# Optimization experiments

Measured on AMD Instinct MI355X. Metric: run time of the kernel, lower is better.

Reference implementation:

```python
import jax, jax.numpy as jnp
import numpy as np

N, M1, M2, D, S0, S1 = 60000, 40000, 40000, 64, 10, 20

def setup_inputs() -> dict:
    key = jax.random.key(0)
    ks = jax.random.split(key, 10)
    return {
        "h0": jax.random.normal(ks[0], (N, D), jnp.float32),
        "h1": jax.random.normal(ks[1], (M1, D), jnp.float32),
        "h2": jax.random.normal(ks[2], (M2, D), jnp.float32),
        "nei0": jax.random.randint(ks[3], (N, S0), 0, M1),
        "nei1": jax.random.randint(ks[4], (N, S1), 0, M2),
        "att_w0": jax.random.normal(ks[5], (1, 2 * D), jnp.float32) * 0.15,
        "att_w1": jax.random.normal(ks[6], (1, 2 * D), jnp.float32) * 0.15,
        "fc_w": jax.random.normal(ks[7], (D, D), jnp.float32) * 0.15,
        "fc_b": jnp.zeros((D,), jnp.float32),
        "fus_att_w": jax.random.normal(ks[8], (1, D), jnp.float32) * 0.15,
        "glob_att": jax.random.normal(ks[9], (1, D), jnp.float32) * 0.15,
        "gate": jnp.float32(0.8),
    }

def _nei_att(nei, h, h_refer, att_w):
    # F.embedding gather: [N, S, D]
    nei_emb = h[nei]
    d = h.shape[-1]
    # concat([h_refer, nei_emb]) @ att.T == h_refer@a_ref + nei_emb@a_nei
    a_ref, a_nei = att_w[0, :d], att_w[0, d:]
    scores = (h_refer @ a_ref)[:, None] + nei_emb @ a_nei  # [N, S]
    scores = jax.nn.leaky_relu(scores, 0.01)
    w = jax.nn.softmax(scores, axis=1)  # softmax over neighbors
    return jnp.einsum('ns,nsd->nd', w, nei_emb)

def reference(h0, h1, h2, nei0, nei1, att_w0, att_w1, fc_w, fc_b, fus_att_w, glob_att, gate):
    # intra (per neighbor type) attention + elu
    e0 = jax.nn.elu(_nei_att(nei0, h1, h0, att_w0))
    e1 = jax.nn.elu(_nei_att(nei1, h2, h0, att_w1))
    # fus_att (inter-type semantic attention)
    def beta_of(e):
        sp = jnp.tanh(e @ fc_w.T + fc_b)
        return (sp @ fus_att_w[0]).mean()
    beta = jax.nn.softmax(jnp.stack([beta_of(e0), beta_of(e1)]))
    z_mc = beta[0] * e0 + beta[1] * e1
    # global encoder: softmax over all nodes of all types
    all_nodes = jnp.concatenate([h0, h1, h2], axis=0)
    s = (all_nodes @ glob_att[0]) / jnp.sqrt(jnp.float32(D))
    w = jax.nn.softmax(s, axis=0)[:, None]
    global_embed = (w * all_nodes).sum(axis=0)  # [D]
    # weighted gate fusion
    gv = jax.nn.sigmoid(gate)
    return gv * z_mc + (1.0 - gv) * global_embed
```

## Files before the change

kernel.cpp:

```cpp
#include <hip/hip_runtime.h>
#include <math.h>

#define N_NODES 60000
#define M1_N    40000
#define M2_N    40000
#define DD      64
#define S0_N    10
#define S1_N    20
#define R_TOTAL (N_NODES + M1_N + M2_N)
#define T_H0    (N_NODES / 16)
#define T_H1    (T_H0 + M1_N / 16)
#define T_ALL   (T_H1 + M2_N / 16)
#define PROJ_GRID 1024
#define BETA_GRID 512

typedef __attribute__((ext_vector_type(8))) short short8;
typedef __attribute__((ext_vector_type(4))) float f32x4;

__device__ __forceinline__ float wave_sum(float x) {
#pragma unroll
    for (int o = 32; o >= 1; o >>= 1) x += __shfl_xor(x, o, 64);
    return x;
}
__device__ __forceinline__ float bcast(float v, int l) {
    return __uint_as_float(__builtin_amdgcn_readlane(__float_as_uint(v), l));
}
__device__ __forceinline__ float tanh_fast(float x) {
    return 1.f - 2.f / (__expf(2.f * x) + 1.f);
}
__device__ __forceinline__ unsigned short f2bf(float x) {
    unsigned u = __float_as_uint(x);
    return (unsigned short)((u + 0x7FFFu + ((u >> 16) & 1u)) >> 16);
}
__device__ __forceinline__ float bf2f(unsigned short u) {
    return __uint_as_float(((unsigned)u) << 16);
}

__global__ __launch_bounds__(256) void k_proj(
    const float* __restrict__ h0, const float* __restrict__ h1, const float* __restrict__ h2,
    const float* __restrict__ aw0, const float* __restrict__ aw1, const float* __restrict__ gatt,
    float* __restrict__ part,
    float* __restrict__ p0r0, float* __restrict__ p0r1,
    float* __restrict__ p1, float* __restrict__ p2,
    unsigned short* __restrict__ h1bf, unsigned short* __restrict__ h2bf)
{
    __shared__ float s_wsum[64];
    __shared__ float s_se;
    __shared__ float s_es[4][16];
    const int tid = threadIdx.x, lane = tid & 63, wid = tid >> 6;
    if (tid < 64) s_wsum[tid] = 0.f;
    if (tid == 0) s_se = 0.f;
    __syncthreads();

    const int m = lane & 15, quad = lane >> 4;

    short8 b0, b1;
    {
        const float* vsel = 0;
        if (m == 1) vsel = aw0;
        else if (m == 2) vsel = aw1;
        else if (m == 3) vsel = aw0 + DD;
        else if (m == 4) vsel = aw1 + DD;
        else if (m == 0) vsel = gatt;
#pragma unroll
        for (int j = 0; j < 8; j++) {
            b0[j] = vsel ? (short)f2bf(vsel[quad * 8 + j]) : (short)0;
            b1[j] = vsel ? (short)f2bf(vsel[32 + quad * 8 + j]) : (short)0;
        }
    }

    float wacc0[8], wacc1[8];
#pragma unroll
    for (int j = 0; j < 8; j++) { wacc0[j] = 0.f; wacc1[j] = 0.f; }
    float r_se = 0.f;

    const int gw = blockIdx.x * 4 + wid, nw = gridDim.x * 4;
    for (int tile = gw; tile < T_ALL; tile += nw) {
        const float* src; int rbase, region;
        if (tile < T_H0)      { src = h0; rbase = tile * 16;          region = 0; }
        else if (tile < T_H1) { src = h1; rbase = (tile - T_H0) * 16; region = 1; }
        else                  { src = h2; rbase = (tile - T_H1) * 16; region = 2; }
        const int row = rbase + m;
        const float4* rpa = (const float4*)(src + (size_t)row * DD + quad * 8);
        const float4* rpb = (const float4*)(src + (size_t)row * DD + 32 + quad * 8);
        const float4 va = rpa[0], vb = rpa[1];
        const float4 vc = rpb[0], vd = rpb[1];

        short8 a0, a1;
        a0[0] = (short)f2bf(va.x); a0[1] = (short)f2bf(va.y);
        a0[2] = (short)f2bf(va.z); a0[3] = (short)f2bf(va.w);
        a0[4] = (short)f2bf(vb.x); a0[5] = (short)f2bf(vb.y);
        a0[6] = (short)f2bf(vb.z); a0[7] = (short)f2bf(vb.w);
        a1[0] = (short)f2bf(vc.x); a1[1] = (short)f2bf(vc.y);
        a1[2] = (short)f2bf(vc.z); a1[3] = (short)f2bf(vc.w);
        a1[4] = (short)f2bf(vd.x); a1[5] = (short)f2bf(vd.y);
        a1[6] = (short)f2bf(vd.z); a1[7] = (short)f2bf(vd.w);

        f32x4 c = {0.f, 0.f, 0.f, 0.f};
        c = __builtin_amdgcn_mfma_f32_16x16x32_bf16(a0, b0, c, 0, 0, 0);
        c = __builtin_amdgcn_mfma_f32_16x16x32_bf16(a1, b1, c, 0, 0, 0);

        if (m == 0) {
            float4 e4;
            e4.x = __expf(c[0] * 0.125f); e4.y = __expf(c[1] * 0.125f);
            e4.z = __expf(c[2] * 0.125f); e4.w = __expf(c[3] * 0.125f);
            *(float4*)&s_es[wid][quad * 4] = e4;
        }
        __builtin_amdgcn_wave_barrier();
        const float es = s_es[wid][m];
        r_se += es;
        wacc0[0] = fmaf(es, va.x, wacc0[0]); wacc0[1] = fmaf(es, va.y, wacc0[1]);
        wacc0[2] = fmaf(es, va.z, wacc0[2]); wacc0[3] = fmaf(es, va.w, wacc0[3]);
        wacc0[4] = fmaf(es, vb.x, wacc0[4]); wacc0[5] = fmaf(es, vb.y, wacc0[5]);
        wacc0[6] = fmaf(es, vb.z, wacc0[6]); wacc0[7] = fmaf(es, vb.w, wacc0[7]);
        wacc1[0] = fmaf(es, vc.x, wacc1[0]); wacc1[1] = fmaf(es, vc.y, wacc1[1]);
        wacc1[2] = fmaf(es, vc.z, wacc1[2]); wacc1[3] = fmaf(es, vc.w, wacc1[3]);
        wacc1[4] = fmaf(es, vd.x, wacc1[4]); wacc1[5] = fmaf(es, vd.y, wacc1[5]);
        wacc1[6] = fmaf(es, vd.z, wacc1[6]); wacc1[7] = fmaf(es, vd.w, wacc1[7]);

        if (region == 0) {
            if (m == 1) { float4 t = {c[0], c[1], c[2], c[3]}; *(float4*)(p0r0 + rbase + quad * 4) = t; }
            if (m == 2) { float4 t = {c[0], c[1], c[2], c[3]}; *(float4*)(p0r1 + rbase + quad * 4) = t; }
        } else if (region == 1) {
            if (m == 3) { float4 t = {c[0], c[1], c[2], c[3]}; *(float4*)(p1 + rbase + quad * 4) = t; }
            *(short8*)(h1bf + (size_t)row * DD + quad * 8) = a0;
            *(short8*)(h1bf + (size_t)row * DD + 32 + quad * 8) = a1;
        } else {
            if (m == 4) { float4 t = {c[0], c[1], c[2], c[3]}; *(float4*)(p2 + rbase + quad * 4) = t; }
            *(short8*)(h2bf + (size_t)row * DD + quad * 8) = a0;
            *(short8*)(h2bf + (size_t)row * DD + 32 + quad * 8) = a1;
        }
    }

    r_se *= 0.25f;
#pragma unroll
    for (int o = 1; o <= 8; o <<= 1) {
#pragma unroll
        for (int j = 0; j < 8; j++) {
            wacc0[j] += __shfl_xor(wacc0[j], o, 64);
            wacc1[j] += __shfl_xor(wacc1[j], o, 64);
        }
    }
    if (m == 0) {
#pragma unroll
        for (int j = 0; j < 8; j++) {
            atomicAdd(&s_wsum[quad * 8 + j],      wacc0[j]);
            atomicAdd(&s_wsum[32 + quad * 8 + j], wacc1[j]);
        }
    }
    const float se = wave_sum(r_se);
    if (lane == 0) atomicAdd(&s_se, se);
    __syncthreads();
    if (tid < 64) part[tid * PROJ_GRID + blockIdx.x] = s_wsum[tid];
    if (tid == 64) part[64 * PROJ_GRID + blockIdx.x] = s_se;
}

__global__ __launch_bounds__(256) void k_attn(
    const unsigned short* __restrict__ h1bf,
    const int* __restrict__ nei0, const int* __restrict__ nei1,
    const float* __restrict__ p0r0, const float* __restrict__ p0r1,
    const float* __restrict__ p1,
    unsigned short* __restrict__ e0bf, unsigned short* __restrict__ e1bf)
{
    const int tid = threadIdx.x, lane = tid & 63, wid = tid >> 6;
    const int sub = lane & 15, grp = lane >> 4;
    const bool grp0 = (lane < S0_N);
    const bool grp1 = (lane >= 32) && (lane < 32 + S1_N);
    const int gw = blockIdx.x * 4 + wid;
    const int nw = gridDim.x * 4;
    for (int n = gw; n < N_NODES; n += nw) {
        const float pr0 = p0r0[n];
        const float pr1 = p0r1[n];

        int idx = 0; float w = 0.f;
        if (grp0) idx = nei0[n * S0_N + lane];
        if (grp1) idx = nei1[n * S1_N + (lane - 32)] + M1_N;
        if (grp0 | grp1) {
            float sc = (grp0 ? pr0 : pr1) + p1[idx];
            sc = (sc >= 0.f) ? sc : 0.01f * sc;
            w = __expf(sc);
        }

        int r0[3], r1[5];
#pragma unroll
        for (int j = 0; j < 3; j++) r0[j] = __shfl(idx, 4 * j + grp, 64);
#pragma unroll
        for (int j = 0; j < 5; j++) r1[j] = __shfl(idx, 32 + 4 * j + grp, 64);

        ushort4 u0[3], u1[5];
#pragma unroll
        for (int j = 0; j < 3; j++)
            u0[j] = *(const ushort4*)(h1bf + r0[j] * DD + 4 * sub);
#pragma unroll
        for (int j = 0; j < 5; j++)
            u1[j] = *(const ushort4*)(h1bf + r1[j] * DD + 4 * sub);

        float sv = w;
#pragma unroll
        for (int o = 16; o >= 1; o >>= 1) sv += __shfl_xor(sv, o, 64);
        const float inv0 = 1.f / bcast(sv, 0);
        const float inv1 = 1.f / bcast(sv, 32);

        float w0[3], w1[5];
#pragma unroll
        for (int j = 0; j < 3; j++) w0[j] = __shfl(w, 4 * j + grp, 64);
#pragma unroll
        for (int j = 0; j < 5; j++) w1[j] = __shfl(w, 32 + 4 * j + grp, 64);

        float4 a0 = make_float4(0.f, 0.f, 0.f, 0.f);
#pragma unroll
        for (int j = 0; j < 3; j++) {
            a0.x = fmaf(w0[j], bf2f(u0[j].x), a0.x);
            a0.y = fmaf(w0[j], bf2f(u0[j].y), a0.y);
            a0.z = fmaf(w0[j], bf2f(u0[j].z), a0.z);
            a0.w = fmaf(w0[j], bf2f(u0[j].w), a0.w);
        }
        float4 a1 = make_float4(0.f, 0.f, 0.f, 0.f);
#pragma unroll
        for (int j = 0; j < 5; j++) {
            a1.x = fmaf(w1[j], bf2f(u1[j].x), a1.x);
            a1.y = fmaf(w1[j], bf2f(u1[j].y), a1.y);
            a1.z = fmaf(w1[j], bf2f(u1[j].z), a1.z);
            a1.w = fmaf(w1[j], bf2f(u1[j].w), a1.w);
        }
#pragma unroll
        for (int o = 16; o <= 32; o <<= 1) {
            a0.x += __shfl_xor(a0.x, o, 64); a0.y += __shfl_xor(a0.y, o, 64);
            a0.z += __shfl_xor(a0.z, o, 64); a0.w += __shfl_xor(a0.w, o, 64);
            a1.x += __shfl_xor(a1.x, o, 64); a1.y += __shfl_xor(a1.y, o, 64);
            a1.z += __shfl_xor(a1.z, o, 64); a1.w += __shfl_xor(a1.w, o, 64);
        }
        float4 e0v, e1v;
        e0v.x = a0.x * inv0; e0v.y = a0.y * inv0; e0v.z = a0.z * inv0; e0v.w = a0.w * inv0;
        e1v.x = a1.x * inv1; e1v.y = a1.y * inv1; e1v.z = a1.z * inv1; e1v.w = a1.w * inv1;
        e0v.x = (e0v.x > 0.f) ? e0v.x : (__expf(e0v.x) - 1.f);
        e0v.y = (e0v.y > 0.f) ? e0v.y : (__expf(e0v.y) - 1.f);
        e0v.z = (e0v.z > 0.f) ? e0v.z : (__expf(e0v.z) - 1.f);
        e0v.w = (e0v.w > 0.f) ? e0v.w : (__expf(e0v.w) - 1.f);
        e1v.x = (e1v.x > 0.f) ? e1v.x : (__expf(e1v.x) - 1.f);
        e1v.y = (e1v.y > 0.f) ? e1v.y : (__expf(e1v.y) - 1.f);
        e1v.z = (e1v.z > 0.f) ? e1v.z : (__expf(e1v.z) - 1.f);
        e1v.w = (e1v.w > 0.f) ? e1v.w : (__expf(e1v.w) - 1.f);
        if (grp == 0) {
            ushort4 s; s.x = f2bf(e0v.x); s.y = f2bf(e0v.y); s.z = f2bf(e0v.z); s.w = f2bf(e0v.w);
            *(ushort4*)(e0bf + n * DD + 4 * sub) = s;
        } else if (grp == 1) {
            ushort4 s; s.x = f2bf(e1v.x); s.y = f2bf(e1v.y); s.z = f2bf(e1v.z); s.w = f2bf(e1v.w);
            *(ushort4*)(e1bf + n * DD + 4 * sub) = s;
        }
    }
}

__global__ __launch_bounds__(256) void k_beta(
    const unsigned short* __restrict__ e0bf, const unsigned short* __restrict__ e1bf,
    const float* __restrict__ fcw, const float* __restrict__ fcb,
    const float* __restrict__ fus, float* __restrict__ bpart)
{
    __shared__ float s_part[2];
    const int tid = threadIdx.x, lane = tid & 63, wid = tid >> 6;
    if (tid < 2) s_part[tid] = 0.f;
    const int m = lane & 15, q = lane >> 4;

    short8 bfr[4][2];
    float fb[4], fu[4];
#pragma unroll
    for (int t = 0; t < 4; t++) {
        const float* wrow = fcw + (t * 16 + m) * DD;
#pragma unroll
        for (int h = 0; h < 2; h++) {
            const float* p = wrow + h * 32 + q * 8;
#pragma unroll
            for (int j = 0; j < 8; j++) bfr[t][h][j] = (short)f2bf(p[j]);
        }
        fb[t] = fcb[t * 16 + m];
        fu[t] = fus[t * 16 + m];
    }
    __syncthreads();

    float rb0 = 0.f, rb1 = 0.f;
    const int gw = blockIdx.x * 4 + wid;
    const int nw = gridDim.x * 4;
    for (int tile = gw; tile < N_NODES / 16; tile += nw) {
        const int rowbase = (tile * 16 + m) * DD + q * 8;
        {
            const short8 a0 = *(const short8*)(e0bf + rowbase);
            const short8 a1 = *(const short8*)(e0bf + rowbase + 32);
            f32x4 c[4];
#pragma unroll
            for (int t = 0; t < 4; t++) {
                c[t] = f32x4{0.f, 0.f, 0.f, 0.f};
                c[t] = __builtin_amdgcn_mfma_f32_16x16x32_bf16(a0, bfr[t][0], c[t], 0, 0, 0);
                c[t] = __builtin_amdgcn_mfma_f32_16x16x32_bf16(a1, bfr[t][1], c[t], 0, 0, 0);
            }
#pragma unroll
            for (int t = 0; t < 4; t++)
#pragma unroll
                for (int j = 0; j < 4; j++)
                    rb0 += tanh_fast(c[t][j] + fb[t]) * fu[t];
        }
        {
            const short8 a0 = *(const short8*)(e1bf + rowbase);
            const short8 a1 = *(const short8*)(e1bf + rowbase + 32);
            f32x4 c[4];
#pragma unroll
            for (int t = 0; t < 4; t++) {
                c[t] = f32x4{0.f, 0.f, 0.f, 0.f};
                c[t] = __builtin_amdgcn_mfma_f32_16x16x32_bf16(a0, bfr[t][0], c[t], 0, 0, 0);
                c[t] = __builtin_amdgcn_mfma_f32_16x16x32_bf16(a1, bfr[t][1], c[t], 0, 0, 0);
            }
#pragma unroll
            for (int t = 0; t < 4; t++)
#pragma unroll
                for (int j = 0; j < 4; j++)
                    rb1 += tanh_fast(c[t][j] + fb[t]) * fu[t];
        }
    }
    const float b0 = wave_sum(rb0);
    const float b1 = wave_sum(rb1);
    if (lane == 0) { atomicAdd(&s_part[0], b0); atomicAdd(&s_part[1], b1); }
    __syncthreads();
    if (tid == 0) {
        bpart[blockIdx.x]             = s_part[0];
        bpart[BETA_GRID + blockIdx.x] = s_part[1];
    }
}

__global__ __launch_bounds__(256) void k_reduce(
    const float* __restrict__ part, const float* __restrict__ bpart,
    float* __restrict__ accum)
{
    const int tid = threadIdx.x, lane = tid & 63, wid = tid >> 6;
    if (wid == 0) {
        float t0 = 0.f, t1 = 0.f;
#pragma unroll
        for (int k = 0; k < BETA_GRID / 64; k++) {
            t0 += bpart[lane + 64 * k];
            t1 += bpart[BETA_GRID + lane + 64 * k];
        }
        t0 = wave_sum(t0); t1 = wave_sum(t1);
        if (lane == 0) { accum[0] = t0; accum[1] = t1; }
    }
    for (int j = wid; j < 65; j += 4) {
        float s = 0.f;
#pragma unroll
        for (int k = 0; k < PROJ_GRID / 64; k++)
            s += part[j * PROJ_GRID + lane + 64 * k];
        s = wave_sum(s);
        if (lane == 0) {
            if (j < 64) accum[4 + j] = s;
            else        accum[2] = s;
        }
    }
}

__global__ __launch_bounds__(256) void k_out(
    const unsigned short* __restrict__ e0bf, const unsigned short* __restrict__ e1bf,
    const float* __restrict__ accum, const float* __restrict__ gate,
    float* __restrict__ out)
{
    const int i = blockIdx.x * 256 + threadIdx.x;
    const float b0 = accum[0] * (1.f / N_NODES);
    const float b1 = accum[1] * (1.f / N_NODES);
    const float mx = fmaxf(b0, b1);
    const float eb0 = __expf(b0 - mx), eb1 = __expf(b1 - mx);
    const float gv  = 1.f / (1.f + __expf(-gate[0]));
    const float c0  = gv * eb0 / (eb0 + eb1);
    const float c1  = gv * eb1 / (eb0 + eb1);
    const float cg  = (1.f - gv) / accum[2];

    const float4 av = ((const float4*)(accum + 4))[i & 15];
    const ushort4 ua = ((const ushort4*)e0bf)[i];
    const ushort4 ub = ((const ushort4*)e1bf)[i];
    float4 o;
    o.x = c0 * bf2f(ua.x) + c1 * bf2f(ub.x) + cg * av.x;
    o.y = c0 * bf2f(ua.y) + c1 * bf2f(ub.y) + cg * av.y;
    o.z = c0 * bf2f(ua.z) + c1 * bf2f(ub.z) + cg * av.z;
    o.w = c0 * bf2f(ua.w) + c1 * bf2f(ub.w) + cg * av.w;
    ((float4*)out)[i] = o;
}

extern "C" void kernel_launch(void* const* d_in, const int* in_sizes, int n_in,
                              void* d_out, int out_size, void* d_ws, size_t ws_size,
                              hipStream_t stream) {
    (void)in_sizes; (void)n_in; (void)out_size; (void)ws_size;
    const float* h0   = (const float*)d_in[0];
    const float* h1   = (const float*)d_in[1];
    const float* h2   = (const float*)d_in[2];
    const int*   nei0 = (const int*)  d_in[3];
    const int*   nei1 = (const int*)  d_in[4];
    const float* aw0  = (const float*)d_in[5];
    const float* aw1  = (const float*)d_in[6];
    const float* fcw  = (const float*)d_in[7];
    const float* fcb  = (const float*)d_in[8];
    const float* fus  = (const float*)d_in[9];
    const float* gatt = (const float*)d_in[10];
    const float* gate = (const float*)d_in[11];
    float* out = (float*)d_out;

    float* ws    = (float*)d_ws;
    float* accum = ws;
    float* p0r0  = ws + 256;
    float* p0r1  = p0r0 + N_NODES;
    float* p1    = p0r1 + N_NODES;
    float* p2    = p1 + M1_N;
    unsigned short* h1bf = (unsigned short*)(p2 + M2_N);
    unsigned short* h2bf = h1bf + (size_t)M1_N * DD;
    unsigned short* e0bf = h2bf + (size_t)M2_N * DD;
    unsigned short* e1bf = e0bf + (size_t)N_NODES * DD;
    float* part  = (float*)(e1bf + (size_t)N_NODES * DD);
    float* bpart = part + 65 * PROJ_GRID;

    k_proj<<<PROJ_GRID, 256, 0, stream>>>(h0, h1, h2, aw0, aw1, gatt, part,
                                          p0r0, p0r1, p1, p2, h1bf, h2bf);
    k_attn<<<2048, 256, 0, stream>>>(h1bf, nei0, nei1, p0r0, p0r1, p1, e0bf, e1bf);
    k_beta<<<BETA_GRID, 256, 0, stream>>>(e0bf, e1bf, fcw, fcb, fus, bpart);
    k_reduce<<<1, 256, 0, stream>>>(part, bpart, accum);
    k_out<<<(N_NODES * DD / 4) / 256, 256, 0, stream>>>(e0bf, e1bf, accum, gate, out);
}
```

Measured before the change: 176.1 us.

## Split neighbor attention into per-type passes, use shuffles for softmax weights

The attention kernel now processes the two neighbor types in separate sweeps over nodes, so each pass gathers from only one table's rows. This is meant to shrink the working set in cache and drop the combined per-node bookkeeping, at the cost of reading the node loop twice. The projection kernel replaces the LDS stage plus wave barrier for exp scores with lane shuffles, which makes every lane compute its own exp. The projection grid is also doubled, which increases the number of partial sums to reduce.

Measured after the change: 182.3 us. 3.5% more time.

```diff
diff --git a/kernel.cpp b/kernel.cpp
--- a/kernel.cpp
+++ b/kernel.cpp
@@ -11,7 +11,7 @@
 #define T_H0    (N_NODES / 16)
 #define T_H1    (T_H0 + M1_N / 16)
 #define T_ALL   (T_H1 + M2_N / 16)
-#define PROJ_GRID 1024
+#define PROJ_GRID 2048
 #define BETA_GRID 512
 
 typedef __attribute__((ext_vector_type(8))) short short8;
@@ -46,7 +46,6 @@
 {
     __shared__ float s_wsum[64];
     __shared__ float s_se;
-    __shared__ float s_es[4][16];
     const int tid = threadIdx.x, lane = tid & 63, wid = tid >> 6;
     if (tid < 64) s_wsum[tid] = 0.f;
     if (tid == 0) s_se = 0.f;
@@ -73,6 +72,9 @@
 #pragma unroll
     for (int j = 0; j < 8; j++) { wacc0[j] = 0.f; wacc1[j] = 0.f; }
     float r_se = 0.f;
+
+    const int srcl = (m >> 2) << 4;
+    const int rsel = m & 3;
 
     const int gw = blockIdx.x * 4 + wid, nw = gridDim.x * 4;
     for (int tile = gw; tile < T_ALL; tile += nw) {
@@ -100,14 +102,12 @@
         c = __builtin_amdgcn_mfma_f32_16x16x32_bf16(a0, b0, c, 0, 0, 0);
         c = __builtin_amdgcn_mfma_f32_16x16x32_bf16(a1, b1, c, 0, 0, 0);
 
-        if (m == 0) {
-            float4 e4;
-            e4.x = __expf(c[0] * 0.125f); e4.y = __expf(c[1] * 0.125f);
-            e4.z = __expf(c[2] * 0.125f); e4.w = __expf(c[3] * 0.125f);
-            *(float4*)&s_es[wid][quad * 4] = e4;
-        }
-        __builtin_amdgcn_wave_barrier();
-        const float es = s_es[wid][m];
+        const float t0 = __shfl(c[0], srcl, 64);
+        const float t1 = __shfl(c[1], srcl, 64);
+        const float t2 = __shfl(c[2], srcl, 64);
+        const float t3 = __shfl(c[3], srcl, 64);
+        const float scr = (rsel == 0) ? t0 : (rsel == 1) ? t1 : (rsel == 2) ? t2 : t3;
+        const float es = __expf(scr * 0.125f);
         r_se += es;
         wacc0[0] = fmaf(es, va.x, wacc0[0]); wacc0[1] = fmaf(es, va.y, wacc0[1]);
         wacc0[2] = fmaf(es, va.z, wacc0[2]); wacc0[3] = fmaf(es, va.w, wacc0[3]);
@@ -164,33 +164,71 @@
 {
     const int tid = threadIdx.x, lane = tid & 63, wid = tid >> 6;
     const int sub = lane & 15, grp = lane >> 4;
-    const bool grp0 = (lane < S0_N);
-    const bool grp1 = (lane >= 32) && (lane < 32 + S1_N);
     const int gw = blockIdx.x * 4 + wid;
     const int nw = gridDim.x * 4;
+
     for (int n = gw; n < N_NODES; n += nw) {
-        const float pr0 = p0r0[n];
-        const float pr1 = p0r1[n];
-
         int idx = 0; float w = 0.f;
-        if (grp0) idx = nei0[n * S0_N + lane];
-        if (grp1) idx = nei1[n * S1_N + (lane - 32)] + M1_N;
-        if (grp0 | grp1) {
-            float sc = (grp0 ? pr0 : pr1) + p1[idx];
+        if (lane < S0_N) {
+            idx = nei0[n * S0_N + lane];
+            float sc = p0r0[n] + p1[idx];
             sc = (sc >= 0.f) ? sc : 0.01f * sc;
             w = __expf(sc);
         }
-
-        int r0[3], r1[5];
+        int r0[3];
 #pragma unroll
         for (int j = 0; j < 3; j++) r0[j] = __shfl(idx, 4 * j + grp, 64);
-#pragma unroll
-        for (int j = 0; j < 5; j++) r1[j] = __shfl(idx, 32 + 4 * j + grp, 64);
-
-        ushort4 u0[3], u1[5];
+        ushort4 u0[3];
 #pragma unroll
         for (int j = 0; j < 3; j++)
             u0[j] = *(const ushort4*)(h1bf + r0[j] * DD + 4 * sub);
+
+        float sv = w;
+#pragma unroll
+        for (int o = 8; o >= 1; o >>= 1) sv += __shfl_xor(sv, o, 64);
+        const float inv = 1.f / bcast(sv, 0);
+
+        float w0[3];
+#pragma unroll
+        for (int j = 0; j < 3; j++) w0[j] = __shfl(w, 4 * j + grp, 64);
+
+        float4 a = make_float4(0.f, 0.f, 0.f, 0.f);
+#pragma unroll
+        for (int j = 0; j < 3; j++) {
+            a.x = fmaf(w0[j], bf2f(u0[j].x), a.x);
+            a.y = fmaf(w0[j], bf2f(u0[j].y), a.y);
+            a.z = fmaf(w0[j], bf2f(u0[j].z), a.z);
+            a.w = fmaf(w0[j], bf2f(u0[j].w), a.w);
+        }
+#pragma unroll
+        for (int o = 16; o <= 32; o <<= 1) {
+            a.x += __shfl_xor(a.x, o, 64); a.y += __shfl_xor(a.y, o, 64);
+            a.z += __shfl_xor(a.z, o, 64); a.w += __shfl_xor(a.w, o, 64);
+        }
+        if (grp == 0) {
+            float4 e;
+            e.x = a.x * inv; e.y = a.y * inv; e.z = a.z * inv; e.w = a.w * inv;
+            e.x = (e.x > 0.f) ? e.x : (__expf(e.x) - 1.f);
+            e.y = (e.y > 0.f) ? e.y : (__expf(e.y) - 1.f);
+            e.z = (e.z > 0.f) ? e.z : (__expf(e.z) - 1.f);
+            e.w = (e.w > 0.f) ? e.w : (__expf(e.w) - 1.f);
+            ushort4 s; s.x = f2bf(e.x); s.y = f2bf(e.y); s.z = f2bf(e.z); s.w = f2bf(e.w);
+            *(ushort4*)(e0bf + n * DD + 4 * sub) = s;
+        }
+    }
+
+    for (int n = gw; n < N_NODES; n += nw) {
+        int idx = 0; float w = 0.f;
+        if (lane < S1_N) {
+            idx = nei1[n * S1_N + lane] + M1_N;
+            float sc = p0r1[n] + p1[idx];
+            sc = (sc >= 0.f) ? sc : 0.01f * sc;
+            w = __expf(sc);
+        }
+        int r1[5];
+#pragma unroll
+        for (int j = 0; j < 5; j++) r1[j] = __shfl(idx, 4 * j + grp, 64);
+        ushort4 u1[5];
 #pragma unroll
         for (int j = 0; j < 5; j++)
             u1[j] = *(const ushort4*)(h1bf + r1[j] * DD + 4 * sub);
@@ -198,54 +236,33 @@
         float sv = w;
 #pragma unroll
         for (int o = 16; o >= 1; o >>= 1) sv += __shfl_xor(sv, o, 64);
-        const float inv0 = 1.f / bcast(sv, 0);
-        const float inv1 = 1.f / bcast(sv, 32);
-
-        float w0[3], w1[5];
-#pragma unroll
-        for (int j = 0; j < 3; j++) w0[j] = __shfl(w, 4 * j + grp, 64);
-#pragma unroll
-        for (int j = 0; j < 5; j++) w1[j] = __shfl(w, 32 + 4 * j + grp, 64);
-
-        float4 a0 = make_float4(0.f, 0.f, 0.f, 0.f);
-#pragma unroll
-        for (int j = 0; j < 3; j++) {
-            a0.x = fmaf(w0[j], bf2f(u0[j].x), a0.x);
-            a0.y = fmaf(w0[j], bf2f(u0[j].y), a0.y);
-            a0.z = fmaf(w0[j], bf2f(u0[j].z), a0.z);
-            a0.w = fmaf(w0[j], bf2f(u0[j].w), a0.w);
-        }
-        float4 a1 = make_float4(0.f, 0.f, 0.f, 0.f);
+        const float inv = 1.f / bcast(sv, 0);
+
+        float w1[5];
+#pragma unroll
+        for (int j = 0; j < 5; j++) w1[j] = __shfl(w, 4 * j + grp, 64);
+
+        float4 a = make_float4(0.f, 0.f, 0.f, 0.f);
 #pragma unroll
         for (int j = 0; j < 5; j++) {
-            a1.x = fmaf(w1[j], bf2f(u1[j].x), a1.x);
-            a1.y = fmaf(w1[j], bf2f(u1[j].y), a1.y);
-            a1.z = fmaf(w1[j], bf2f(u1[j].z), a1.z);
-            a1.w = fmaf(w1[j], bf2f(u1[j].w), a1.w);
+            a.x = fmaf(w1[j], bf2f(u1[j].x), a.x);
+            a.y = fmaf(w1[j], bf2f(u1[j].y), a.y);
+            a.z = fmaf(w1[j], bf2f(u1[j].z), a.z);
+            a.w = fmaf(w1[j], bf2f(u1[j].w), a.w);
         }
 #pragma unroll
         for (int o = 16; o <= 32; o <<= 1) {
-            a0.x += __shfl_xor(a0.x, o, 64); a0.y += __shfl_xor(a0.y, o, 64);
-            a0.z += __shfl_xor(a0.z, o, 64); a0.w += __shfl_xor(a0.w, o, 64);
-            a1.x += __shfl_xor(a1.x, o, 64); a1.y += __shfl_xor(a1.y, o, 64);
-            a1.z += __shfl_xor(a1.z, o, 64); a1.w += __shfl_xor(a1.w, o, 64);
-        }
-        float4 e0v, e1v;
-        e0v.x = a0.x * inv0; e0v.y = a0.y * inv0; e0v.z = a0.z * inv0; e0v.w = a0.w * inv0;
-        e1v.x = a1.x * inv1; e1v.y = a1.y * inv1; e1v.z = a1.z * inv1; e1v.w = a1.w * inv1;
-        e0v.x = (e0v.x > 0.f) ? e0v.x : (__expf(e0v.x) - 1.f);
-        e0v.y = (e0v.y > 0.f) ? e0v.y : (__expf(e0v.y) - 1.f);
-        e0v.z = (e0v.z > 0.f) ? e0v.z : (__expf(e0v.z) - 1.f);
-        e0v.w = (e0v.w > 0.f) ? e0v.w : (__expf(e0v.w) - 1.f);
-        e1v.x = (e1v.x > 0.f) ? e1v.x : (__expf(e1v.x) - 1.f);
-        e1v.y = (e1v.y > 0.f) ? e1v.y : (__expf(e1v.y) - 1.f);
-        e1v.z = (e1v.z > 0.f) ? e1v.z : (__expf(e1v.z) - 1.f);
-        e1v.w = (e1v.w > 0.f) ? e1v.w : (__expf(e1v.w) - 1.f);
+            a.x += __shfl_xor(a.x, o, 64); a.y += __shfl_xor(a.y, o, 64);
+            a.z += __shfl_xor(a.z, o, 64); a.w += __shfl_xor(a.w, o, 64);
+        }
         if (grp == 0) {
-            ushort4 s; s.x = f2bf(e0v.x); s.y = f2bf(e0v.y); s.z = f2bf(e0v.z); s.w = f2bf(e0v.w);
-            *(ushort4*)(e0bf + n * DD + 4 * sub) = s;
-        } else if (grp == 1) {
-            ushort4 s; s.x = f2bf(e1v.x); s.y = f2bf(e1v.y); s.z = f2bf(e1v.z); s.w = f2bf(e1v.w);
+            float4 e;
+            e.x = a.x * inv; e.y = a.y * inv; e.z = a.z * inv; e.w = a.w * inv;
+            e.x = (e.x > 0.f) ? e.x : (__expf(e.x) - 1.f);
+            e.y = (e.y > 0.f) ? e.y : (__expf(e.y) - 1.f);
+            e.z = (e.z > 0.f) ? e.z : (__expf(e.z) - 1.f);
+            e.w = (e.w > 0.f) ? e.w : (__expf(e.w) - 1.f);
+            ushort4 s; s.x = f2bf(e.x); s.y = f2bf(e.y); s.z = f2bf(e.z); s.w = f2bf(e.w);
             *(ushort4*)(e1bf + n * DD + 4 * sub) = s;
         }
     }
```
